# Performance work log

Hardware: AMD Instinct MI355X
Metric: run time of the kernel (lower is better)

## Reference

```python
import jax, jax.numpy as jnp
import numpy as np

N_NODES = 50000
C = 256          # in_channels == hidden_size
E = 800000


def setup_inputs() -> dict:
    key = jax.random.key(0)
    ks = jax.random.split(key, 12)
    x = jax.random.normal(ks[0], (N_NODES, C), dtype=jnp.float32)
    edge_index = jax.random.randint(ks[1], (2, E), 0, N_NODES, dtype=jnp.int64)
    edge_attr = jax.random.uniform(ks[2], (E,), dtype=jnp.float32)
    edge_weights_index = jax.random.randint(ks[3], (2, E), 0, N_NODES, dtype=jnp.int64)
    s = 1.0 / np.sqrt(C)
    # TopKPooling projection vector
    p_pool = jax.random.normal(ks[4], (C,), dtype=jnp.float32) * s
    # GRU (input=C, hidden=C): gates stacked [r, z, n]
    W_ih = jax.random.normal(ks[5], (3 * C, C), dtype=jnp.float32) * s
    W_hh = jax.random.normal(ks[6], (3 * C, C), dtype=jnp.float32) * s
    b_ih = jnp.zeros((3 * C,), dtype=jnp.float32)
    b_hh = jnp.zeros((3 * C,), dtype=jnp.float32)
    # initial evolving GCN weight [C, C]
    W_init = jax.random.normal(ks[7], (C, C), dtype=jnp.float32) * s
    # EdgeDecoder MLP
    lin1_w = jax.random.normal(ks[8], (C, 2 * C), dtype=jnp.float32) / np.sqrt(2 * C)
    lin1_b = jnp.zeros((C,), dtype=jnp.float32)
    lin2_w = jax.random.normal(ks[9], (1, C), dtype=jnp.float32) * s
    lin2_b = jnp.zeros((1,), dtype=jnp.float32)
    return {
        "x": x, "edge_index": edge_index, "edge_attr": edge_attr,
        "edge_weights_index": edge_weights_index,
        "p_pool": p_pool, "W_ih": W_ih, "W_hh": W_hh, "b_ih": b_ih, "b_hh": b_hh,
        "W_init": W_init, "lin1_w": lin1_w, "lin1_b": lin1_b,
        "lin2_w": lin2_w, "lin2_b": lin2_b,
    }


def _forward(x, edge_attr, p_pool, W_ih, W_hh, b_ih, b_hh, W_init,
             lin1_w, lin1_b, lin2_w, lin2_b, edge_index, edge_weights_index):
    n_nodes, c = x.shape
    # --- EvolveGCNH: TopK pooling summary (k = in_channels) ---
    score = x @ p_pool / jnp.linalg.norm(p_pool)          # [N]
    top_score, perm = jax.lax.top_k(score, c)             # [C]
    x_tilde = x[perm] * jnp.tanh(top_score)[:, None]      # [C, C]
    # --- GRU step: input x_tilde (batch=C), hidden = evolving weight W_init ---
    gi = x_tilde @ W_ih.T + b_ih                           # [C, 3C]
    gh = W_init @ W_hh.T + b_hh                            # [C, 3C]
    i_r, i_z, i_n = jnp.split(gi, 3, axis=1)
    h_r, h_z, h_n = jnp.split(gh, 3, axis=1)
    r = jax.nn.sigmoid(i_r + h_r)
    z = jax.nn.sigmoid(i_z + h_z)
    n = jnp.tanh(i_n + r * h_n)
    W = (1.0 - z) * n + z * W_init                         # [C, C] evolved GCN weight
    # --- GCNConv with fixed W, add_self_loops=False ---
    xw = x @ W                                             # [N, C]
    src, dst = edge_index[0], edge_index[1]
    deg = jax.ops.segment_sum(edge_attr, dst, num_segments=n_nodes)
    dinv = jnp.where(deg > 0, jax.lax.rsqrt(jnp.where(deg > 0, deg, 1.0)), 0.0)
    norm = dinv[src] * edge_attr * dinv[dst]               # [E]
    node_emb = jax.ops.segment_sum(xw[src] * norm[:, None], dst,
                                   num_segments=n_nodes)   # [N, C]
    # --- EdgeDecoder: gather src/trg, concat, MLP ---
    s_idx, t_idx = edge_weights_index[0], edge_weights_index[1]
    edge_emb = jnp.concatenate([node_emb[s_idx], node_emb[t_idx]], axis=1)  # [E, 2C]
    h = jax.nn.relu(edge_emb @ lin1_w.T + lin1_b)          # [E, C]
    pred = h @ lin2_w.T + lin2_b                           # [E, 1]
    return pred.reshape(-1)


def reference(x, edge_index, edge_attr, edge_weights_index, p_pool,
              W_ih, W_hh, b_ih, b_hh, W_init, lin1_w, lin1_b, lin2_w, lin2_b):
    # dropout is identity in eval mode
    return _forward(x, edge_attr, p_pool, W_ih, W_hh, b_ih, b_hh, W_init,
                    lin1_w, lin1_b, lin2_w, lin2_b, edge_index, edge_weights_index)
```

## Files before the change

### kernel.cpp

```cpp
#include <hip/hip_runtime.h>
#include <hip/hip_bf16.h>
#include <math.h>


typedef __attribute__((ext_vector_type(8))) short bf16x8;
typedef __attribute__((ext_vector_type(8))) unsigned short u16x8;
typedef __attribute__((ext_vector_type(4))) float f32x4;

#define WSHIFT 9
#define WMASK 511
#define NBUCK 98

__device__ __forceinline__ unsigned f2key(float f) {
  unsigned u = __float_as_uint(f);
  return (u & 0x80000000u) ? ~u : (u | 0x80000000u);
}

__device__ __forceinline__ unsigned short f2bf(float f) {
  unsigned u = __float_as_uint(f);
  unsigned r = u + 0x7fffu + ((u >> 16) & 1u);
  return (unsigned short)(r >> 16);
}
__device__ __forceinline__ float bf2f(unsigned short h) {
  return __uint_as_float((unsigned)h << 16);
}

template <int CTRL>
__device__ __forceinline__ float dpp_add(float s) {
  int t = __builtin_amdgcn_update_dpp(0, __float_as_int(s), CTRL, 0xf, 0xf, false);
  return s + __int_as_float(t);
}

__device__ __forceinline__ void gload16(const void* g, void* l) {
  __builtin_amdgcn_global_load_lds((const __attribute__((address_space(1))) void*)g,
                                   (__attribute__((address_space(3))) void*)l, 16, 0, 0);
}

__global__ __launch_bounds__(256) void fusedA_kernel(const float* __restrict__ x,
                                                     const float* __restrict__ p,
                                                     float* __restrict__ score,
                                                     unsigned short* __restrict__ xh, int N, int NS,
                                                     const int* __restrict__ ei,
                                                     const int* __restrict__ ewi,
                                                     int* __restrict__ bh1p,
                                                     int* __restrict__ bh2p, int E,
                                                     const float* __restrict__ lin1,
                                                     unsigned short* __restrict__ WAB) {
  int tid = threadIdx.x;
  int b = blockIdx.x;
  if (b < NS) {
    int node = b * 4 + (tid >> 6);
    int lane = tid & 63;
    if (node >= N) return;
    float4 xv = ((const float4*)(x + (size_t)node * 256))[lane];
    ushort4 hv;
    hv.x = f2bf(xv.x);
    hv.y = f2bf(xv.y);
    hv.z = f2bf(xv.z);
    hv.w = f2bf(xv.w);
    ((ushort4*)(xh + (size_t)node * 256))[lane] = hv;
    float4 pv = ((const float4*)p)[lane];
    float s = xv.x * pv.x + xv.y * pv.y + xv.z * pv.z + xv.w * pv.w;
    float sp = pv.x * pv.x + pv.y * pv.y + pv.z * pv.z + pv.w * pv.w;
#pragma unroll
    for (int off = 32; off > 0; off >>= 1) {
      s += __shfl_down(s, off, 64);
      sp += __shfl_down(sp, off, 64);
    }
    if (lane == 0) score[node] = s / sqrtf(sp);
  } else if (b < NS + 64) {
    __shared__ int c1[128], c2[128];
    int bb = b - NS;
    if (tid < 128) { c1[tid] = 0; c2[tid] = 0; }
    __syncthreads();
    int idx = bb * 256 + tid;
    int stride = 64 * 256;
    for (int e = idx; e < E; e += stride) {
      atomicAdd(&c1[ei[E + e] >> WSHIFT], 1);
      atomicAdd(&c2[ewi[e] >> WSHIFT], 1);
    }
    __syncthreads();
    if (tid < 128) {
      bh1p[bb * 128 + tid] = c1[tid];
      bh2p[bb * 128 + tid] = c2[tid];
    }
  } else {
    int idx = (b - NS - 64) * 256 + tid;
    int n = idx >> 9, k = idx & 511;
    unsigned short h = f2bf(lin1[idx]);
    if (k < 256)
      WAB[n * 256 + k] = h;
    else
      WAB[(256 + n) * 256 + (k - 256)] = h;
  }
}

__global__ __launch_bounds__(256) void fusedB_kernel(const float* __restrict__ score, int n,
                                                     int* __restrict__ ghp,
                                                     const int* __restrict__ bh1p,
                                                     const int* __restrict__ bh2p,
                                                     int* __restrict__ bbase1,
                                                     int* __restrict__ bbase2,
                                                     int* __restrict__ gcur1,
                                                     int* __restrict__ gcur2,
                                                     int* __restrict__ rowp1,
                                                     int* __restrict__ rowp2, int N, int E) {
  int tid = threadIdx.x;
  if (blockIdx.x < 64) {
    __shared__ int lh[4096];
    for (int i = tid; i < 4096; i += 256) lh[i] = 0;
    __syncthreads();
    int idx = blockIdx.x * 256 + tid;
    int stride = 64 * 256;
    for (int i = idx; i < n; i += stride) {
      unsigned key = f2key(score[i]);
      atomicAdd(&lh[key >> 20], 1);
    }
    __syncthreads();
    int* row = ghp + blockIdx.x * 4096;
    for (int i = tid; i < 4096; i += 256) row[i] = lh[i];
  } else {
    __shared__ int ss[128];
    __shared__ int pp[256];
    int bk = tid & 127, hf = tid >> 7;
    {
      int vp = 0;
      if (bk < NBUCK)
        for (int r = hf * 32; r < hf * 32 + 32; ++r) vp += bh1p[r * 128 + bk];
      pp[tid] = vp;
    }
    __syncthreads();
    int v = 0;
    if (tid < 128) { v = pp[tid] + pp[tid + 128]; ss[tid] = v; }
    __syncthreads();
    for (int off = 1; off < 128; off <<= 1) {
      int a = 0, bsum = 0;
      if (tid < 128) { a = ss[tid]; bsum = (tid >= off) ? ss[tid - off] : 0; }
      __syncthreads();
      if (tid < 128) ss[tid] = a + bsum;
      __syncthreads();
    }
    if (tid < 128) {
      int excl = ss[tid] - v;
      if (tid < NBUCK) { bbase1[tid] = excl; gcur1[tid] = excl; }
      if (tid == NBUCK - 1) bbase1[NBUCK] = excl + v;
    }
    __syncthreads();
    {
      int vp = 0;
      if (bk < NBUCK)
        for (int r = hf * 32; r < hf * 32 + 32; ++r) vp += bh2p[r * 128 + bk];
      pp[tid] = vp;
    }
    __syncthreads();
    int v2 = 0;
    if (tid < 128) { v2 = pp[tid] + pp[tid + 128]; ss[tid] = v2; }
    __syncthreads();
    for (int off = 1; off < 128; off <<= 1) {
      int a = 0, bsum = 0;
      if (tid < 128) { a = ss[tid]; bsum = (tid >= off) ? ss[tid - off] : 0; }
      __syncthreads();
      if (tid < 128) ss[tid] = a + bsum;
      __syncthreads();
    }
    if (tid < 128) {
      int excl = ss[tid] - v2;
      if (tid < NBUCK) { bbase2[tid] = excl; gcur2[tid] = excl; }
      if (tid == NBUCK - 1) bbase2[NBUCK] = excl + v2;
    }
    if (tid == 0) { rowp1[N] = E; rowp2[N] = E; }
  }
}

__global__ __launch_bounds__(1024) void fusedC_kernel(const int* __restrict__ ei,
                                                      const float* __restrict__ attr,
                                                      int* __restrict__ gcur1,
                                                      int2* __restrict__ stage1,
                                                      const int* __restrict__ ewi,
                                                      int* __restrict__ gcur2,
                                                      int2* __restrict__ stage2,
                                                      int E, int nb,
                                                      const float* __restrict__ score, int n, int k,
                                                      const int* __restrict__ ghp,
                                                      int* __restrict__ perm,
                                                      float* __restrict__ tts) {
  int tid = threadIdx.x;
  if ((int)blockIdx.x < 2 * nb) {
    bool conv = (int)blockIdx.x < nb;
    __shared__ int pcnt[128], pcur[128];
    int base = (conv ? blockIdx.x : blockIdx.x - nb) * 8192;
    int* gcur = conv ? gcur1 : gcur2;
    int2* stage = conv ? stage1 : stage2;
    if (tid < 128) pcnt[tid] = 0;
    __syncthreads();
    int bk[8];
    int2 pl[8];
#pragma unroll
    for (int i = 0; i < 8; ++i) {
      int e = base + i * 1024 + tid;
      bk[i] = -1;
      if (e < E) {
        if (conv) {
          int d = ei[E + e];
          int s = ei[e];
          bk[i] = d >> WSHIFT;
          pl[i] = make_int2(s | ((d & WMASK) << 16), __float_as_int(attr[e]));
        } else {
          int s = ewi[e];
          int d = ewi[E + e];
          bk[i] = s >> WSHIFT;
          pl[i] = make_int2(d | ((s & WMASK) << 16), e);
        }
        atomicAdd(&pcnt[bk[i]], 1);
      }
    }
    __syncthreads();
    if (tid < NBUCK) {
      int c = pcnt[tid];
      pcur[tid] = c ? atomicAdd(&gcur[tid], c) : 0;
    }
    __syncthreads();
#pragma unroll
    for (int i = 0; i < 8; ++i) {
      if (bk[i] >= 0) {
        int pos = atomicAdd(&pcur[bk[i]], 1);
        stage[pos] = pl[i];
      }
    }
  } else {
    __shared__ int part[1024];
    __shared__ unsigned sT;
    int s0, s1, s2, s3;
    {
      int b0 = tid * 4;
      s0 = 0; s1 = 0; s2 = 0; s3 = 0;
      for (int r = 0; r < 64; ++r) {
        int4 v4 = *(const int4*)(ghp + r * 4096 + b0);
        s0 += v4.x; s1 += v4.y; s2 += v4.z; s3 += v4.w;
      }
      part[tid] = s0 + s1 + s2 + s3;
      __syncthreads();
      for (int off = 1; off < 1024; off <<= 1) {
        int v = part[tid];
        int add = (tid + off < 1024) ? part[tid + off] : 0;
        __syncthreads();
        part[tid] = v + add;
        __syncthreads();
      }
      int sufChunk = part[tid];
      int sufNext = (tid < 1023) ? part[tid + 1] : 0;
      if (sufNext < k && sufChunk >= k) {
        int run = sufNext;
        int b;
        run += s3;
        if (run >= k) b = tid * 4 + 3;
        else {
          run += s2;
          if (run >= k) b = tid * 4 + 2;
          else {
            run += s1;
            b = (run >= k) ? tid * 4 + 1 : tid * 4;
          }
        }
        sT = ((unsigned)b) << 20;
      }
    }
    __syncthreads();
    unsigned T = sT;
    __shared__ unsigned keys[1024];
    __shared__ int idxs[1024];
    __shared__ int cnt;
    if (tid == 0) cnt = 0;
    keys[tid] = 0u;
    idxs[tid] = 0x7fffffff;
    __syncthreads();
    for (int i = tid; i < n; i += 1024) {
      unsigned key = f2key(score[i]);
      if (key >= T) {
        int p = atomicAdd(&cnt, 1);
        if (p < 1024) { keys[p] = key; idxs[p] = i; }
      }
    }
    __syncthreads();
    for (int size = 2; size <= 1024; size <<= 1) {
      for (int stride = size >> 1; stride > 0; stride >>= 1) {
        int j = tid ^ stride;
        if (j > tid) {
          unsigned ka = keys[tid], kb = keys[j];
          int ia = idxs[tid], ib = idxs[j];
          bool aBefore = (ka > kb) || (ka == kb && ia < ib);
          bool up = ((tid & size) == 0);
          if (aBefore != up) {
            keys[tid] = kb; keys[j] = ka;
            idxs[tid] = ib; idxs[j] = ia;
          }
        }
        __syncthreads();
      }
    }
    if (tid < k) {
      int idx = idxs[tid];
      perm[tid] = idx;
      tts[tid] = tanhf(score[idx]);
    }
  }
}

__global__ __launch_bounds__(256) void fusedD_kernel(const float* __restrict__ x,
                                                     const int* __restrict__ perm,
                                                     const float* __restrict__ tts,
                                                     const float* __restrict__ Wi,
                                                     const float* __restrict__ W_ih,
                                                     const float* __restrict__ W_hh,
                                                     const float* __restrict__ b_ih,
                                                     const float* __restrict__ b_hh,
                                                     unsigned short* __restrict__ Wr,
                                                     const int2* __restrict__ stage1,
                                                     const int* __restrict__ bbase1,
                                                     int2* __restrict__ esv,
                                                     int* __restrict__ rowp1,
                                                     float* __restrict__ dinv,
                                                     const int2* __restrict__ stage2,
                                                     const int* __restrict__ bbase2,
                                                     int2* __restrict__ eto,
                                                     int* __restrict__ rowp2, int N) {
  int tid = threadIdx.x;
  if (blockIdx.x < 256) {
    int i = blockIdx.x, j = tid;
    __shared__ float sx[256], sh[256];
    sx[j] = x[(size_t)perm[i] * 256 + j] * tts[i];
    sh[j] = Wi[i * 256 + j];
    __syncthreads();
    float gi[3], gh[3];
#pragma unroll
    for (int g = 0; g < 3; ++g) {
      int row = g * 256 + j;
      const float4* wi4 = (const float4*)(W_ih + (size_t)row * 256);
      const float4* wh4 = (const float4*)(W_hh + (size_t)row * 256);
      float si = 0.f, s2 = 0.f;
      for (int k4 = 0; k4 < 64; ++k4) {
        float4 wv = wi4[k4];
        float4 hv = wh4[k4];
        int k = k4 * 4;
        si += sx[k] * wv.x + sx[k + 1] * wv.y + sx[k + 2] * wv.z + sx[k + 3] * wv.w;
        s2 += sh[k] * hv.x + sh[k + 1] * hv.y + sh[k + 2] * hv.z + sh[k + 3] * hv.w;
      }
      gi[g] = si + b_ih[row];
      gh[g] = s2 + b_hh[row];
    }
    float r = 1.f / (1.f + expf(-(gi[0] + gh[0])));
    float z = 1.f / (1.f + expf(-(gi[1] + gh[1])));
    float nn = tanhf(gi[2] + r * gh[2]);
    float w = (1.f - z) * nn + z * sh[j];
    Wr[(size_t)i * 256 + j] = f2bf(w);
  } else {
    __shared__ int cnt[512];
    __shared__ float degs[512];
    __shared__ int pref[512];
    __shared__ int ss[256];
    int bb2 = blockIdx.x - 256;
    bool isConv = bb2 < NBUCK;
    int b = isConv ? bb2 : bb2 - NBUCK;
    const int2* stage = isConv ? stage1 : stage2;
    const int* bbase = isConv ? bbase1 : bbase2;
    int beg = bbase[b], end = bbase[b + 1];
    int node0 = b << WSHIFT;
    cnt[tid] = 0; cnt[tid + 256] = 0;
    degs[tid] = 0.f; degs[tid + 256] = 0.f;
    __syncthreads();
    for (int j = beg + tid; j < end; j += 256) {
      int2 p = stage[j];
      int loc = p.x >> 16;
      atomicAdd(&cnt[loc], 1);
      if (isConv) atomicAdd(&degs[loc], __int_as_float(p.y));
    }
    __syncthreads();
    int c0 = cnt[2 * tid], c1 = cnt[2 * tid + 1];
    ss[tid] = c0 + c1;
    __syncthreads();
    for (int off = 1; off < 256; off <<= 1) {
      int a = ss[tid];
      int bsum = (tid >= off) ? ss[tid - off] : 0;
      __syncthreads();
      ss[tid] = a + bsum;
      __syncthreads();
    }
    int excl = (tid ? ss[tid - 1] : 0);
    pref[2 * tid] = excl;
    pref[2 * tid + 1] = excl + c0;
    __syncthreads();
#pragma unroll
    for (int h = 0; h < 2; ++h) {
      int i = tid + h * 256;
      int node = node0 + i;
      if (node < N) {
        if (isConv) {
          rowp1[node] = beg + pref[i];
          float d = degs[i];
          dinv[node] = d > 0.f ? 1.f / sqrtf(d) : 0.f;
        } else {
          rowp2[node] = beg + pref[i];
        }
      }
    }
    __syncthreads();
    int2* outb = isConv ? esv : eto;
    for (int j = beg + tid; j < end; j += 256) {
      int2 p = stage[j];
      int loc = p.x >> 16;
      int pos = beg + atomicAdd(&pref[loc], 1);
      outb[pos] = make_int2(p.x & 0xFFFF, p.y);
    }
  }
}

__global__ __launch_bounds__(256) void fusedE_kernel(const unsigned short* __restrict__ xh,
                                                     const int* __restrict__ row_ptr,
                                                     const int2* __restrict__ esv,
                                                     const float* __restrict__ dinv,
                                                     unsigned short* __restrict__ agg, int N, int NSB,
                                                     const unsigned short* __restrict__ WAB,
                                                     const unsigned short* __restrict__ Wr,
                                                     unsigned short* __restrict__ PAB) {
  int tid = threadIdx.x;
  int lane = tid & 63;
  if ((int)blockIdx.x >= NSB) {
    int cb = blockIdx.x - NSB;
    int by = cb >> 4;
    int mbase = (cb & 15) * 16;
    int wave = tid >> 6;
    int quad = lane >> 4, r16 = lane & 15;
    int n0 = wave * 64;
    const unsigned short* A = WAB + ((size_t)by << 16);
    f32x4 acc[4];
#pragma unroll
    for (int j = 0; j < 4; ++j) acc[j] = (f32x4){0.f, 0.f, 0.f, 0.f};
    for (int k0 = 0; k0 < 256; k0 += 32) {
      int koff = k0 + quad * 8;
      bf16x8 af = *(const bf16x8*)(A + (size_t)(mbase + r16) * 256 + koff);
#pragma unroll
      for (int nt = 0; nt < 4; ++nt) {
        bf16x8 bfr = *(const bf16x8*)(Wr + (size_t)(n0 + nt * 16 + r16) * 256 + koff);
        acc[nt] = __builtin_amdgcn_mfma_f32_16x16x32_bf16(af, bfr, acc[nt], 0, 0, 0);
      }
    }
#pragma unroll
    for (int rr = 0; rr < 4; ++rr) {
      int grow = mbase + quad * 4 + rr;
#pragma unroll
      for (int nt = 0; nt < 4; ++nt)
        PAB[(size_t)(by * 256 + grow) * 256 + n0 + nt * 16 + r16] = f2bf(acc[nt][rr]);
    }
    return;
  }
  int node = blockIdx.x * 4 + (tid >> 6);
  int g = lane & 15, q = lane >> 4;
  if (node >= N) return;
  int beg = row_ptr[node], end = row_ptr[node + 1];
  float acc[16];
#pragma unroll
  for (int c = 0; c < 16; ++c) acc[c] = 0.f;
  const unsigned short* xb = xh + g * 16;

  for (int cb = beg; cb < end; cb += 64) {
    int cend = cb + 64 < end ? cb + 64 : end;
    int me = cb + lane;
    int2 mm = (me < cend) ? esv[me] : make_int2(0, 0);
    int mx = mm.x;
    float mv = __int_as_float(mm.y) * dinv[mx];

    float vA = 0.f, vB = 0.f, vC = 0.f;
    u16x8 rAa, rAb, rBa, rBb, rCa, rCb;
    {
      int e = cb + q;
      int sx = __shfl(mx, q, 64);
      float tv = __shfl(mv, q, 64);
      vA = (e < cend) ? tv : 0.f;
      rAa = *(const u16x8*)(xb + (size_t)sx * 256);
      rAb = *(const u16x8*)(xb + (size_t)sx * 256 + 8);
    }
    if (cb + 4 < cend) {
      int e = cb + 4 + q;
      int sx = __shfl(mx, 4 + q, 64);
      float tv = __shfl(mv, 4 + q, 64);
      vB = (e < cend) ? tv : 0.f;
      rBa = *(const u16x8*)(xb + (size_t)sx * 256);
      rBb = *(const u16x8*)(xb + (size_t)sx * 256 + 8);
    } else { rBa = rAa; rBb = rAb; }
    if (cb + 8 < cend) {
      int e = cb + 8 + q;
      int sx = __shfl(mx, 8 + q, 64);
      float tv = __shfl(mv, 8 + q, 64);
      vC = (e < cend) ? tv : 0.f;
      rCa = *(const u16x8*)(xb + (size_t)sx * 256);
      rCb = *(const u16x8*)(xb + (size_t)sx * 256 + 8);
    } else { rCa = rAa; rCb = rAb; }

    for (int jb = cb; jb < cend; jb += 12) {
#pragma unroll
      for (int c = 0; c < 8; ++c) acc[c] += bf2f(rAa[c]) * vA;
#pragma unroll
      for (int c = 0; c < 8; ++c) acc[8 + c] += bf2f(rAb[c]) * vA;
      vA = 0.f;
      if (jb + 12 < cend) {
        int e = jb + 12 + q;
        int idx = (e - cb) & 63;
        int sx = __shfl(mx, idx, 64);
        float tv = __shfl(mv, idx, 64);
        vA = (e < cend) ? tv : 0.f;
        rAa = *(const u16x8*)(xb + (size_t)sx * 256);
        rAb = *(const u16x8*)(xb + (size_t)sx * 256 + 8);
      }
#pragma unroll
      for (int c = 0; c < 8; ++c) acc[c] += bf2f(rBa[c]) * vB;
#pragma unroll
      for (int c = 0; c < 8; ++c) acc[8 + c] += bf2f(rBb[c]) * vB;
      vB = 0.f;
      if (jb + 16 < cend) {
        int e = jb + 16 + q;
        int idx = (e - cb) & 63;
        int sx = __shfl(mx, idx, 64);
        float tv = __shfl(mv, idx, 64);
        vB = (e < cend) ? tv : 0.f;
        rBa = *(const u16x8*)(xb + (size_t)sx * 256);
        rBb = *(const u16x8*)(xb + (size_t)sx * 256 + 8);
      }
#pragma unroll
      for (int c = 0; c < 8; ++c) acc[c] += bf2f(rCa[c]) * vC;
#pragma unroll
      for (int c = 0; c < 8; ++c) acc[8 + c] += bf2f(rCb[c]) * vC;
      vC = 0.f;
      if (jb + 20 < cend) {
        int e = jb + 20 + q;
        int idx = (e - cb) & 63;
        int sx = __shfl(mx, idx, 64);
        float tv = __shfl(mv, idx, 64);
        vC = (e < cend) ? tv : 0.f;
        rCa = *(const u16x8*)(xb + (size_t)sx * 256);
        rCb = *(const u16x8*)(xb + (size_t)sx * 256 + 8);
      }
    }
  }
#pragma unroll
  for (int c = 0; c < 16; ++c) {
    acc[c] += __shfl_xor(acc[c], 16, 64);
    acc[c] += __shfl_xor(acc[c], 32, 64);
  }
  if (q == 0) {
    float dd = dinv[node];
    u16x8 o0, o1;
#pragma unroll
    for (int c = 0; c < 8; ++c) {
      o0[c] = f2bf(acc[c] * dd);
      o1[c] = f2bf(acc[8 + c] * dd);
    }
    *(u16x8*)(agg + (size_t)node * 256 + g * 16) = o0;
    *(u16x8*)(agg + (size_t)node * 256 + g * 16 + 8) = o1;
  }
}

__global__ __launch_bounds__(512) void mfma_gemm128(const unsigned short* __restrict__ A,
                                                    const unsigned short* __restrict__ BT,
                                                    unsigned short* __restrict__ C1,
                                                    unsigned short* __restrict__ C2,
                                                    int M) {
  __shared__ unsigned short sA[128 * 32];
  __shared__ unsigned short sB[256 * 32];
  int tid = threadIdx.x;
  int wave = tid >> 6, lane = tid & 63;
  int quad = lane >> 4, r16 = lane & 15;
  int wm = wave >> 2, wn = wave & 3;
  int mbase = blockIdx.x * 128;
  const unsigned short* Bt = BT + ((size_t)blockIdx.y << 16);
  unsigned short* Cout = blockIdx.y ? C2 : C1;

  int srow = tid >> 2, scolq = tid & 3;
  const unsigned short* gA = A + (size_t)(mbase + srow) * 256 + scolq * 8;
  const unsigned short* gB0 = Bt + (size_t)srow * 256 + scolq * 8;
  const unsigned short* gB1 = Bt + (size_t)(128 + srow) * 256 + scolq * 8;
  unsigned short* lA = sA + wave * 512;
  unsigned short* lB0 = sB + wave * 512;
  unsigned short* lB1 = sB + 4096 + wave * 512;

  f32x4 acc[4][4];
#pragma unroll
  for (int i = 0; i < 4; ++i)
#pragma unroll
    for (int j = 0; j < 4; ++j) acc[i][j] = (f32x4){0.f, 0.f, 0.f, 0.f};

  const unsigned short* pA = sA + (wm * 64 + r16) * 32 + quad * 8;
  const unsigned short* pB = sB + (wn * 64 + r16) * 32 + quad * 8;

  for (int k0 = 0; k0 < 256; k0 += 32) {
    if (k0) __syncthreads();
    gload16(gA + k0, lA);
    gload16(gB0 + k0, lB0);
    gload16(gB1 + k0, lB1);
    __syncthreads();
    bf16x8 af[4], bfr[4];
#pragma unroll
    for (int mt = 0; mt < 4; ++mt) af[mt] = *(const bf16x8*)(pA + mt * 512);
#pragma unroll
    for (int nt = 0; nt < 4; ++nt) bfr[nt] = *(const bf16x8*)(pB + nt * 512);
#pragma unroll
    for (int mt = 0; mt < 4; ++mt)
#pragma unroll
      for (int nt = 0; nt < 4; ++nt)
        acc[mt][nt] = __builtin_amdgcn_mfma_f32_16x16x32_bf16(af[mt], bfr[nt], acc[mt][nt], 0, 0, 0);
  }
#pragma unroll
  for (int mt = 0; mt < 4; ++mt) {
#pragma unroll
    for (int rr = 0; rr < 4; ++rr) {
      int grow = mbase + wm * 64 + mt * 16 + quad * 4 + rr;
      if (grow < M) {
#pragma unroll
        for (int nt = 0; nt < 4; ++nt)
          Cout[(size_t)grow * 256 + wn * 64 + nt * 16 + r16] = f2bf(acc[mt][nt][rr]);
      }
    }
  }
}

__global__ __launch_bounds__(256) void edge_decode_csr(const unsigned short* __restrict__ A,
                                                       const unsigned short* __restrict__ Bm,
                                                       const int* __restrict__ row_ptr,
                                                       const int2* __restrict__ eto,
                                                       const float* __restrict__ b1,
                                                       const float* __restrict__ w2,
                                                       const float* __restrict__ b2,
                                                       float* __restrict__ out, int N) {
  int node = blockIdx.x * 4 + (threadIdx.x >> 6);
  int lane = threadIdx.x & 63;
  int g = lane & 15, q = lane >> 4;
  if (node >= N) return;
  int beg = row_ptr[node], end = row_ptr[node + 1];
  if (beg >= end) return;
  float a[16], w[16];
  {
    u16x8 a0 = *(const u16x8*)(A + (size_t)node * 256 + g * 16);
    u16x8 a1 = *(const u16x8*)(A + (size_t)node * 256 + g * 16 + 8);
    const float4* bp = (const float4*)(b1 + g * 16);
    const float4* wp = (const float4*)(w2 + g * 16);
#pragma unroll
    for (int i = 0; i < 4; ++i) {
      float4 bv = bp[i];
      float4 wv = wp[i];
      a[i * 4 + 0] = (i < 2 ? bf2f(a0[i * 4 + 0]) : bf2f(a1[i * 4 - 8])) + bv.x;
      a[i * 4 + 1] = (i < 2 ? bf2f(a0[i * 4 + 1]) : bf2f(a1[i * 4 - 7])) + bv.y;
      a[i * 4 + 2] = (i < 2 ? bf2f(a0[i * 4 + 2]) : bf2f(a1[i * 4 - 6])) + bv.z;
      a[i * 4 + 3] = (i < 2 ? bf2f(a0[i * 4 + 3]) : bf2f(a1[i * 4 - 5])) + bv.w;
      w[i * 4 + 0] = wv.x;
      w[i * 4 + 1] = wv.y;
      w[i * 4 + 2] = wv.z;
      w[i * 4 + 3] = wv.w;
    }
  }
  float base = b2[0];
  const unsigned short* Bb = Bm + g * 16;

  for (int cb = beg; cb < end; cb += 64) {
    int cend = cb + 64 < end ? cb + 64 : end;
    int me = cb + lane;
    int2 mm = (me < cend) ? eto[me] : make_int2(0, 0);
    int mx = mm.x, my = mm.y;

    bool okA = false, okB = false, okC = false;
    int oA = 0, oB = 0, oC = 0;
    u16x8 rAa, rAb, rBa, rBb, rCa, rCb;
    {
      int e = cb + q;
      int sx = __shfl(mx, q, 64);
      oA = __shfl(my, q, 64);
      okA = e < cend;
      rAa = *(const u16x8*)(Bb + (size_t)sx * 256);
      rAb = *(const u16x8*)(Bb + (size_t)sx * 256 + 8);
    }
    if (cb + 4 < cend) {
      int e = cb + 4 + q;
      int sx = __shfl(mx, 4 + q, 64);
      oB = __shfl(my, 4 + q, 64);
      okB = e < cend;
      rBa = *(const u16x8*)(Bb + (size_t)sx * 256);
      rBb = *(const u16x8*)(Bb + (size_t)sx * 256 + 8);
    } else { rBa = rAa; rBb = rAb; }
    if (cb + 8 < cend) {
      int e = cb + 8 + q;
      int sx = __shfl(mx, 8 + q, 64);
      oC = __shfl(my, 8 + q, 64);
      okC = e < cend;
      rCa = *(const u16x8*)(Bb + (size_t)sx * 256);
      rCb = *(const u16x8*)(Bb + (size_t)sx * 256 + 8);
    } else { rCa = rAa; rCb = rAb; }

    for (int jb = cb; jb < cend; jb += 12) {
      {
        float s0 = 0.f, s1 = 0.f;
#pragma unroll
        for (int c = 0; c < 8; ++c) s0 += fmaxf(a[c] + bf2f(rAa[c]), 0.f) * w[c];
#pragma unroll
        for (int c = 0; c < 8; ++c) s1 += fmaxf(a[8 + c] + bf2f(rAb[c]), 0.f) * w[8 + c];
        float s = s0 + s1;
        s = dpp_add<0x128>(s);
        s = dpp_add<0x124>(s);
        s = dpp_add<0x122>(s);
        s = dpp_add<0x121>(s);
        if (g == 0 && okA) out[oA] = s + base;
      }
      okA = false;
      if (jb + 12 < cend) {
        int e = jb + 12 + q;
        int idx = (e - cb) & 63;
        int sx = __shfl(mx, idx, 64);
        oA = __shfl(my, idx, 64);
        okA = e < cend;
        rAa = *(const u16x8*)(Bb + (size_t)sx * 256);
        rAb = *(const u16x8*)(Bb + (size_t)sx * 256 + 8);
      }
      {
        float s0 = 0.f, s1 = 0.f;
#pragma unroll
        for (int c = 0; c < 8; ++c) s0 += fmaxf(a[c] + bf2f(rBa[c]), 0.f) * w[c];
#pragma unroll
        for (int c = 0; c < 8; ++c) s1 += fmaxf(a[8 + c] + bf2f(rBb[c]), 0.f) * w[8 + c];
        float s = s0 + s1;
        s = dpp_add<0x128>(s);
        s = dpp_add<0x124>(s);
        s = dpp_add<0x122>(s);
        s = dpp_add<0x121>(s);
        if (g == 0 && okB) out[oB] = s + base;
      }
      okB = false;
      if (jb + 16 < cend) {
        int e = jb + 16 + q;
        int idx = (e - cb) & 63;
        int sx = __shfl(mx, idx, 64);
        oB = __shfl(my, idx, 64);
        okB = e < cend;
        rBa = *(const u16x8*)(Bb + (size_t)sx * 256);
        rBb = *(const u16x8*)(Bb + (size_t)sx * 256 + 8);
      }
      {
        float s0 = 0.f, s1 = 0.f;
#pragma unroll
        for (int c = 0; c < 8; ++c) s0 += fmaxf(a[c] + bf2f(rCa[c]), 0.f) * w[c];
#pragma unroll
        for (int c = 0; c < 8; ++c) s1 += fmaxf(a[8 + c] + bf2f(rCb[c]), 0.f) * w[8 + c];
        float s = s0 + s1;
        s = dpp_add<0x128>(s);
        s = dpp_add<0x124>(s);
        s = dpp_add<0x122>(s);
        s = dpp_add<0x121>(s);
        if (g == 0 && okC) out[oC] = s + base;
      }
      okC = false;
      if (jb + 20 < cend) {
        int e = jb + 20 + q;
        int idx = (e - cb) & 63;
        int sx = __shfl(mx, idx, 64);
        oC = __shfl(my, idx, 64);
        okC = e < cend;
        rCa = *(const u16x8*)(Bb + (size_t)sx * 256);
        rCb = *(const u16x8*)(Bb + (size_t)sx * 256 + 8);
      }
    }
  }
}

extern "C" void kernel_launch(void* const* d_in, const int* in_sizes, int n_in,
                              void* d_out, int out_size, void* d_ws, size_t ws_size,
                              hipStream_t stream) {
  const float* x      = (const float*)d_in[0];
  const int*   ei     = (const int*)d_in[1];
  const float* attr   = (const float*)d_in[2];
  const int*   ewi    = (const int*)d_in[3];
  const float* p_pool = (const float*)d_in[4];
  const float* W_ih   = (const float*)d_in[5];
  const float* W_hh   = (const float*)d_in[6];
  const float* b_ih   = (const float*)d_in[7];
  const float* b_hh   = (const float*)d_in[8];
  const float* W_init = (const float*)d_in[9];
  const float* lin1_w = (const float*)d_in[10];
  const float* lin1_b = (const float*)d_in[11];
  const float* lin2_w = (const float*)d_in[12];
  const float* lin2_b = (const float*)d_in[13];
  float* out = (float*)d_out;

  const int C = 256;
  const int N = in_sizes[0] / C;
  const int E = in_sizes[2];

  char* ws = (char*)d_ws;
  size_t off = 0;
  auto alloc = [&](size_t bytes) {
    size_t o = off;
    off = (off + bytes + 255) & ~(size_t)255;
    return o;
  };
  float*          score  = (float*)(ws + alloc((size_t)N * 4));
  int*            perm   = (int*)(ws + alloc(C * 4));
  float*          tts    = (float*)(ws + alloc(C * 4));
  unsigned short* Wr     = (unsigned short*)(ws + alloc((size_t)C * C * 2));
  unsigned short* WAB    = (unsigned short*)(ws + alloc((size_t)2 * C * C * 2));
  unsigned short* PAB    = (unsigned short*)(ws + alloc((size_t)2 * C * C * 2));
  int*            bh1p   = (int*)(ws + alloc((size_t)64 * 128 * 4));
  int*            bh2p   = (int*)(ws + alloc((size_t)64 * 128 * 4));
  int*            ghp    = (int*)(ws + alloc((size_t)64 * 4096 * 4));
  int*            bbase1 = (int*)(ws + alloc((NBUCK + 1) * 4));
  int*            bbase2 = (int*)(ws + alloc((NBUCK + 1) * 4));
  int*            gcur1  = (int*)(ws + alloc(128 * 4));
  int*            gcur2  = (int*)(ws + alloc(128 * 4));
  float*          dinv   = (float*)(ws + alloc((size_t)N * 4));
  int*            rowp1  = (int*)(ws + alloc((size_t)(N + 1) * 4));
  int*            rowp2  = (int*)(ws + alloc((size_t)(N + 1) * 4));
  int2*           stage1 = (int2*)(ws + alloc((size_t)E * 8));
  int2*           stage2 = (int2*)(ws + alloc((size_t)E * 8));
  int2*           esv    = (int2*)(ws + alloc((size_t)E * 8));
  int2*           eto    = (int2*)(ws + alloc((size_t)E * 8));
  unsigned short* xh     = (unsigned short*)(ws + alloc((size_t)N * C * 2));
  unsigned short* agg    = (unsigned short*)(ws + alloc((size_t)N * C * 2));
  unsigned short* Bbf    = (unsigned short*)(ws + alloc((size_t)N * C * 2));
  unsigned short* Abf = xh;

  int NS = (N + 3) / 4;
  int nbP1 = (E + 8191) / 8192;

  fusedA_kernel<<<NS + 64 + 512, 256, 0, stream>>>(x, p_pool, score, xh, N, NS,
                                                   ei, ewi, bh1p, bh2p, E,
                                                   lin1_w, WAB);

  fusedB_kernel<<<65, 256, 0, stream>>>(score, N, ghp, bh1p, bh2p,
                                        bbase1, bbase2, gcur1, gcur2,
                                        rowp1, rowp2, N, E);

  fusedC_kernel<<<2 * nbP1 + 1, 1024, 0, stream>>>(ei, attr, gcur1, stage1,
                                                   ewi, gcur2, stage2, E, nbP1,
                                                   score, N, C, ghp, perm, tts);

  fusedD_kernel<<<256 + 2 * NBUCK, 256, 0, stream>>>(x, perm, tts, W_init,
                                                     W_ih, W_hh, b_ih, b_hh, Wr,
                                                     stage1, bbase1, esv, rowp1, dinv,
                                                     stage2, bbase2, eto, rowp2, N);

  fusedE_kernel<<<NS + 32, 256, 0, stream>>>(xh, rowp1, esv, dinv, agg, N, NS,
                                             WAB, Wr, PAB);

  mfma_gemm128<<<dim3((N + 127) / 128, 2), 512, 0, stream>>>(agg, PAB, Abf, Bbf, N);

  edge_decode_csr<<<NS, 256, 0, stream>>>(Abf, Bbf, rowp2, eto,
                                          lin1_b, lin2_w, lin2_b, out, N);
}
```

Measured before the change: 419.6 us.

## Compute x·W before aggregation and drop the fused lin1·W weight product

The evolved GCN weight is now written transposed, and a full-size MFMA GEMM computes xw = x·W first. The CSR gather then aggregates xw, and the decoder GEMM runs directly against the bf16 lin1 weights. This replaces the earlier order: aggregate raw x, then multiply by a precomputed product of lin1 and W. The change adds one N×256×256 GEMM pass and one kernel launch, and removes the small weight-product kernel branch. The edge-histogram blocks in the first fused kernel are also moved ahead of the per-node scoring blocks so that they get scheduled early.

Measured after the change: 432.2 us. 1.03x slower.

```diff
diff --git a/kernel.cpp b/kernel.cpp
--- a/kernel.cpp
+++ b/kernel.cpp
@@ -48,8 +48,23 @@
                                                      unsigned short* __restrict__ WAB) {
   int tid = threadIdx.x;
   int b = blockIdx.x;
-  if (b < NS) {
-    int node = b * 4 + (tid >> 6);
+  if (b < 64) {
+    __shared__ int c1[128], c2[128];
+    if (tid < 128) { c1[tid] = 0; c2[tid] = 0; }
+    __syncthreads();
+    int idx = b * 256 + tid;
+    int stride = 64 * 256;
+    for (int e = idx; e < E; e += stride) {
+      atomicAdd(&c1[ei[E + e] >> WSHIFT], 1);
+      atomicAdd(&c2[ewi[e] >> WSHIFT], 1);
+    }
+    __syncthreads();
+    if (tid < 128) {
+      bh1p[b * 128 + tid] = c1[tid];
+      bh2p[b * 128 + tid] = c2[tid];
+    }
+  } else if (b < 64 + NS) {
+    int node = (b - 64) * 4 + (tid >> 6);
     int lane = tid & 63;
     if (node >= N) return;
     float4 xv = ((const float4*)(x + (size_t)node * 256))[lane];
@@ -68,24 +83,8 @@
       sp += __shfl_down(sp, off, 64);
     }
     if (lane == 0) score[node] = s / sqrtf(sp);
-  } else if (b < NS + 64) {
-    __shared__ int c1[128], c2[128];
-    int bb = b - NS;
-    if (tid < 128) { c1[tid] = 0; c2[tid] = 0; }
-    __syncthreads();
-    int idx = bb * 256 + tid;
-    int stride = 64 * 256;
-    for (int e = idx; e < E; e += stride) {
-      atomicAdd(&c1[ei[E + e] >> WSHIFT], 1);
-      atomicAdd(&c2[ewi[e] >> WSHIFT], 1);
-    }
-    __syncthreads();
-    if (tid < 128) {
-      bh1p[bb * 128 + tid] = c1[tid];
-      bh2p[bb * 128 + tid] = c2[tid];
-    }
   } else {
-    int idx = (b - NS - 64) * 256 + tid;
+    int idx = (b - 64 - NS) * 256 + tid;
     int n = idx >> 9, k = idx & 511;
     unsigned short h = f2bf(lin1[idx]);
     if (k < 256)
@@ -314,7 +313,7 @@
                                                      const float* __restrict__ W_hh,
                                                      const float* __restrict__ b_ih,
                                                      const float* __restrict__ b_hh,
-                                                     unsigned short* __restrict__ Wr,
+                                                     unsigned short* __restrict__ WevoT,
                                                      const int2* __restrict__ stage1,
                                                      const int* __restrict__ bbase1,
                                                      int2* __restrict__ esv,
@@ -352,7 +351,7 @@
     float z = 1.f / (1.f + expf(-(gi[1] + gh[1])));
     float nn = tanhf(gi[2] + r * gh[2]);
     float w = (1.f - z) * nn + z * sh[j];
-    Wr[(size_t)i * 256 + j] = f2bf(w);
+    WevoT[(size_t)j * 256 + i] = f2bf(w);
   } else {
     __shared__ int cnt[512];
     __shared__ float degs[512];
@@ -414,53 +413,83 @@
   }
 }
 
-__global__ __launch_bounds__(256) void fusedE_kernel(const unsigned short* __restrict__ xh,
-                                                     const int* __restrict__ row_ptr,
-                                                     const int2* __restrict__ esv,
-                                                     const float* __restrict__ dinv,
-                                                     unsigned short* __restrict__ agg, int N, int NSB,
-                                                     const unsigned short* __restrict__ WAB,
-                                                     const unsigned short* __restrict__ Wr,
-                                                     unsigned short* __restrict__ PAB) {
+__global__ __launch_bounds__(512) void mfma_gemm128(const unsigned short* __restrict__ A,
+                                                    const unsigned short* __restrict__ BT,
+                                                    unsigned short* __restrict__ C1,
+                                                    unsigned short* __restrict__ C2,
+                                                    int M) {
+  __shared__ unsigned short sA[128 * 32];
+  __shared__ unsigned short sB[256 * 32];
   int tid = threadIdx.x;
-  int lane = tid & 63;
-  if ((int)blockIdx.x >= NSB) {
-    int cb = blockIdx.x - NSB;
-    int by = cb >> 4;
-    int mbase = (cb & 15) * 16;
-    int wave = tid >> 6;
-    int quad = lane >> 4, r16 = lane & 15;
-    int n0 = wave * 64;
-    const unsigned short* A = WAB + ((size_t)by << 16);
-    f32x4 acc[4];
-#pragma unroll
-    for (int j = 0; j < 4; ++j) acc[j] = (f32x4){0.f, 0.f, 0.f, 0.f};
-    for (int k0 = 0; k0 < 256; k0 += 32) {
-      int koff = k0 + quad * 8;
-      bf16x8 af = *(const bf16x8*)(A + (size_t)(mbase + r16) * 256 + koff);
-#pragma unroll
-      for (int nt = 0; nt < 4; ++nt) {
-        bf16x8 bfr = *(const bf16x8*)(Wr + (size_t)(n0 + nt * 16 + r16) * 256 + koff);
-        acc[nt] = __builtin_amdgcn_mfma_f32_16x16x32_bf16(af, bfr, acc[nt], 0, 0, 0);
-      }
-    }
+  int wave = tid >> 6, lane = tid & 63;
+  int quad = lane >> 4, r16 = lane & 15;
+  int wm = wave >> 2, wn = wave & 3;
+  int mbase = blockIdx.x * 128;
+  const unsigned short* Bt = BT + ((size_t)blockIdx.y << 16);
+  unsigned short* Cout = blockIdx.y ? C2 : C1;
+
+  int srow = tid >> 2, scolq = tid & 3;
+  const unsigned short* gA = A + (size_t)(mbase + srow) * 256 + scolq * 8;
+  const unsigned short* gB0 = Bt + (size_t)srow * 256 + scolq * 8;
+  const unsigned short* gB1 = Bt + (size_t)(128 + srow) * 256 + scolq * 8;
+  unsigned short* lA = sA + wave * 512;
+  unsigned short* lB0 = sB + wave * 512;
+  unsigned short* lB1 = sB + 4096 + wave * 512;
+
+  f32x4 acc[4][4];
+#pragma unroll
+  for (int i = 0; i < 4; ++i)
+#pragma unroll
+    for (int j = 0; j < 4; ++j) acc[i][j] = (f32x4){0.f, 0.f, 0.f, 0.f};
+
+  const unsigned short* pA = sA + (wm * 64 + r16) * 32 + quad * 8;
+  const unsigned short* pB = sB + (wn * 64 + r16) * 32 + quad * 8;
+
+  for (int k0 = 0; k0 < 256; k0 += 32) {
+    if (k0) __syncthreads();
+    gload16(gA + k0, lA);
+    gload16(gB0 + k0, lB0);
+    gload16(gB1 + k0, lB1);
+    __syncthreads();
+    bf16x8 af[4], bfr[4];
+#pragma unroll
+    for (int mt = 0; mt < 4; ++mt) af[mt] = *(const bf16x8*)(pA + mt * 512);
+#pragma unroll
+    for (int nt = 0; nt < 4; ++nt) bfr[nt] = *(const bf16x8*)(pB + nt * 512);
+#pragma unroll
+    for (int mt = 0; mt < 4; ++mt)
+#pragma unroll
+      for (int nt = 0; nt < 4; ++nt)
+        acc[mt][nt] = __builtin_amdgcn_mfma_f32_16x16x32_bf16(af[mt], bfr[nt], acc[mt][nt], 0, 0, 0);
+  }
+#pragma unroll
+  for (int mt = 0; mt < 4; ++mt) {
 #pragma unroll
     for (int rr = 0; rr < 4; ++rr) {
-      int grow = mbase + quad * 4 + rr;
-#pragma unroll
-      for (int nt = 0; nt < 4; ++nt)
-        PAB[(size_t)(by * 256 + grow) * 256 + n0 + nt * 16 + r16] = f2bf(acc[nt][rr]);
-    }
-    return;
-  }
-  int node = blockIdx.x * 4 + (tid >> 6);
+      int grow = mbase + wm * 64 + mt * 16 + quad * 4 + rr;
+      if (grow < M) {
+#pragma unroll
+        for (int nt = 0; nt < 4; ++nt)
+          Cout[(size_t)grow * 256 + wn * 64 + nt * 16 + r16] = f2bf(acc[mt][nt][rr]);
+      }
+    }
+  }
+}
+
+__global__ __launch_bounds__(256) void gcn_gather(const unsigned short* __restrict__ xw,
+                                                  const int* __restrict__ row_ptr,
+                                                  const int2* __restrict__ esv,
+                                                  const float* __restrict__ dinv,
+                                                  unsigned short* __restrict__ ne, int N) {
+  int node = blockIdx.x * 4 + (threadIdx.x >> 6);
+  int lane = threadIdx.x & 63;
   int g = lane & 15, q = lane >> 4;
   if (node >= N) return;
   int beg = row_ptr[node], end = row_ptr[node + 1];
   float acc[16];
 #pragma unroll
   for (int c = 0; c < 16; ++c) acc[c] = 0.f;
-  const unsigned short* xb = xh + g * 16;
+  const unsigned short* xb = xw + g * 16;
 
   for (int cb = beg; cb < end; cb += 64) {
     int cend = cb + 64 < end ? cb + 64 : end;
@@ -554,71 +583,8 @@
       o0[c] = f2bf(acc[c] * dd);
       o1[c] = f2bf(acc[8 + c] * dd);
     }
-    *(u16x8*)(agg + (size_t)node * 256 + g * 16) = o0;
-    *(u16x8*)(agg + (size_t)node * 256 + g * 16 + 8) = o1;
-  }
-}
-
-__global__ __launch_bounds__(512) void mfma_gemm128(const unsigned short* __restrict__ A,
-                                                    const unsigned short* __restrict__ BT,
-                                                    unsigned short* __restrict__ C1,
-                                                    unsigned short* __restrict__ C2,
-                                                    int M) {
-  __shared__ unsigned short sA[128 * 32];
-  __shared__ unsigned short sB[256 * 32];
-  int tid = threadIdx.x;
-  int wave = tid >> 6, lane = tid & 63;
-  int quad = lane >> 4, r16 = lane & 15;
-  int wm = wave >> 2, wn = wave & 3;
-  int mbase = blockIdx.x * 128;
-  const unsigned short* Bt = BT + ((size_t)blockIdx.y << 16);
-  unsigned short* Cout = blockIdx.y ? C2 : C1;
-
-  int srow = tid >> 2, scolq = tid & 3;
-  const unsigned short* gA = A + (size_t)(mbase + srow) * 256 + scolq * 8;
-  const unsigned short* gB0 = Bt + (size_t)srow * 256 + scolq * 8;
-  const unsigned short* gB1 = Bt + (size_t)(128 + srow) * 256 + scolq * 8;
-  unsigned short* lA = sA + wave * 512;
-  unsigned short* lB0 = sB + wave * 512;
-  unsigned short* lB1 = sB + 4096 + wave * 512;
-
-  f32x4 acc[4][4];
-#pragma unroll
-  for (int i = 0; i < 4; ++i)
-#pragma unroll
-    for (int j = 0; j < 4; ++j) acc[i][j] = (f32x4){0.f, 0.f, 0.f, 0.f};
-
-  const unsigned short* pA = sA + (wm * 64 + r16) * 32 + quad * 8;
-  const unsigned short* pB = sB + (wn * 64 + r16) * 32 + quad * 8;
-
-  for (int k0 = 0; k0 < 256; k0 += 32) {
-    if (k0) __syncthreads();
-    gload16(gA + k0, lA);
-    gload16(gB0 + k0, lB0);
-    gload16(gB1 + k0, lB1);
-    __syncthreads();
-    bf16x8 af[4], bfr[4];
-#pragma unroll
-    for (int mt = 0; mt < 4; ++mt) af[mt] = *(const bf16x8*)(pA + mt * 512);
-#pragma unroll
-    for (int nt = 0; nt < 4; ++nt) bfr[nt] = *(const bf16x8*)(pB + nt * 512);
-#pragma unroll
-    for (int mt = 0; mt < 4; ++mt)
-#pragma unroll
-      for (int nt = 0; nt < 4; ++nt)
-        acc[mt][nt] = __builtin_amdgcn_mfma_f32_16x16x32_bf16(af[mt], bfr[nt], acc[mt][nt], 0, 0, 0);
-  }
-#pragma unroll
-  for (int mt = 0; mt < 4; ++mt) {
-#pragma unroll
-    for (int rr = 0; rr < 4; ++rr) {
-      int grow = mbase + wm * 64 + mt * 16 + quad * 4 + rr;
-      if (grow < M) {
-#pragma unroll
-        for (int nt = 0; nt < 4; ++nt)
-          Cout[(size_t)grow * 256 + wn * 64 + nt * 16 + r16] = f2bf(acc[mt][nt][rr]);
-      }
-    }
+    *(u16x8*)(ne + (size_t)node * 256 + g * 16) = o0;
+    *(u16x8*)(ne + (size_t)node * 256 + g * 16 + 8) = o1;
   }
 }
 
@@ -800,9 +766,8 @@
   float*          score  = (float*)(ws + alloc((size_t)N * 4));
   int*            perm   = (int*)(ws + alloc(C * 4));
   float*          tts    = (float*)(ws + alloc(C * 4));
-  unsigned short* Wr     = (unsigned short*)(ws + alloc((size_t)C * C * 2));
+  unsigned short* WevoT  = (unsigned short*)(ws + alloc((size_t)C * C * 2));
   unsigned short* WAB    = (unsigned short*)(ws + alloc((size_t)2 * C * C * 2));
-  unsigned short* PAB    = (unsigned short*)(ws + alloc((size_t)2 * C * C * 2));
   int*            bh1p   = (int*)(ws + alloc((size_t)64 * 128 * 4));
   int*            bh2p   = (int*)(ws + alloc((size_t)64 * 128 * 4));
   int*            ghp    = (int*)(ws + alloc((size_t)64 * 4096 * 4));
@@ -818,14 +783,15 @@
   int2*           esv    = (int2*)(ws + alloc((size_t)E * 8));
   int2*           eto    = (int2*)(ws + alloc((size_t)E * 8));
   unsigned short* xh     = (unsigned short*)(ws + alloc((size_t)N * C * 2));
-  unsigned short* agg    = (unsigned short*)(ws + alloc((size_t)N * C * 2));
+  unsigned short* xwh    = (unsigned short*)(ws + alloc((size_t)N * C * 2));
   unsigned short* Bbf    = (unsigned short*)(ws + alloc((size_t)N * C * 2));
-  unsigned short* Abf = xh;
+  unsigned short* ne  = xh;
+  unsigned short* Abf = xwh;
 
   int NS = (N + 3) / 4;
   int nbP1 = (E + 8191) / 8192;
 
-  fusedA_kernel<<<NS + 64 + 512, 256, 0, stream>>>(x, p_pool, score, xh, N, NS,
+  fusedA_kernel<<<64 + NS + 512, 256, 0, stream>>>(x, p_pool, score, xh, N, NS,
                                                    ei, ewi, bh1p, bh2p, E,
                                                    lin1_w, WAB);
 
@@ -838,14 +804,15 @@
                                                    score, N, C, ghp, perm, tts);
 
   fusedD_kernel<<<256 + 2 * NBUCK, 256, 0, stream>>>(x, perm, tts, W_init,
-                                                     W_ih, W_hh, b_ih, b_hh, Wr,
+                                                     W_ih, W_hh, b_ih, b_hh, WevoT,
                                                      stage1, bbase1, esv, rowp1, dinv,
                                                      stage2, bbase2, eto, rowp2, N);
 
-  fusedE_kernel<<<NS + 32, 256, 0, stream>>>(xh, rowp1, esv, dinv, agg, N, NS,
-                                             WAB, Wr, PAB);
-
-  mfma_gemm128<<<dim3((N + 127) / 128, 2), 512, 0, stream>>>(agg, PAB, Abf, Bbf, N);
+  mfma_gemm128<<<dim3((N + 127) / 128, 1), 512, 0, stream>>>(xh, WevoT, xwh, xwh, N);
+
+  gcn_gather<<<NS, 256, 0, stream>>>(xwh, rowp1, esv, dinv, ne, N);
+
+  mfma_gemm128<<<dim3((N + 127) / 128, 2), 512, 0, stream>>>(ne, WAB, Abf, Bbf, N);
 
   edge_decode_csr<<<NS, 256, 0, stream>>>(Abf, Bbf, rowp2, eto,
                                           lin1_b, lin2_w, lin2_b, out, N);
```
